# Performance work log

Hardware: AMD Instinct MI355X
Metric: run time of the kernel (lower is better)

## Reference

```python
import jax, jax.numpy as jnp
import numpy as np

BETA = 0.001  # init kwarg beta
S, K = 32768, 32  # segments x candidates-per-segment (uniform segments)


def setup_inputs() -> dict:
    key = jax.random.key(0)
    logits = jax.random.normal(key, (S * K,), dtype=jnp.float32)
    # cumulative segment offsets: [0, K, 2K, ..., S*K]  (uniform ragged structure)
    k_lens = jnp.arange(S + 1, dtype=jnp.int32) * K
    return {"logits": logits, "k_lens": k_lens}


def reference(logits, k_lens):
    # Static shapes derived from array shapes (uniform segments).
    n_seg = k_lens.shape[0] - 1              # S
    seg_len = logits.shape[0] // n_seg       # K
    seg = logits.reshape(n_seg, seg_len)     # [S, K]
    # torch.combinations(arange(K), 2) == upper-triangular index pairs (i < j)
    i_idx, j_idx = jnp.triu_indices(seg_len, k=1)  # each [P], P = K*(K-1)/2
    pos = seg[:, i_idx]                      # [S, P]
    neg = seg[:, j_idx]                      # [S, P]
    l2 = 0.5 * (pos * pos - neg * neg)
    # per-segment loss: -mean(logsigmoid(pos-neg) + beta*l2)
    loss = -jnp.mean(jax.nn.log_sigmoid(pos - neg) + BETA * l2, axis=1)  # [S]
    return loss  # reduction=None -> stacked per-segment losses
```

## Files before the change

### kernel.cpp

```cpp
#include <hip/hip_runtime.h>


constexpr int K = 32;
constexpr int ITERS = 16;

struct alignas(16) Tab {
    unsigned int A[64][4];
    unsigned int B[64][4];
};
constexpr Tab make_tab() {
    Tab t{};
    unsigned char ai[512] = {}, aj[512] = {};
    int p = 0;
    for (int i = 0; i < K; ++i)
        for (int j = i + 1; j < K; ++j) { ai[p] = (unsigned char)(i * 4); aj[p] = (unsigned char)(j * 4); ++p; }
    for (int it = 0; it < ITERS; ++it)
        for (int l = 0; l < 32; ++l) {
            const int s = it * 32 + l;
            for (int half = 0; half < 2; ++half) {
                const int lane = l + 32 * half;
                const unsigned int a = ai[s] + 128u * half;
                const unsigned int b = aj[s] + 128u * half;
                t.A[lane][it >> 2] |= a << ((it & 3) * 8);
                t.B[lane][it >> 2] |= b << ((it & 3) * 8);
            }
        }
    return t;
}
__constant__ Tab TAB = make_tab();

__device__ __forceinline__ float bperm(int byteaddr, float v) {
    return __int_as_float(__builtin_amdgcn_ds_bpermute(byteaddr, __float_as_int(v)));
}

#if __has_builtin(__builtin_amdgcn_exp2f)
#define FAST_EXP2(x) __builtin_amdgcn_exp2f(x)
#else
#define FAST_EXP2(x) exp2f(x)
#endif
#if __has_builtin(__builtin_amdgcn_logf)
#define FAST_LOG2(x) __builtin_amdgcn_logf(x)
#else
#define FAST_LOG2(x) log2f(x)
#endif

__global__ __launch_bounds__(1024) void rmloss_kernel(
        const float* __restrict__ logits, float* __restrict__ out, int n_seg) {
    const int lane = threadIdx.x & 63;
    const int wave = blockIdx.x * 16 + (threadIdx.x >> 6);
    const int seg0 = wave * 2;
    if (seg0 >= n_seg) return;

    const long long gidx = (long long)wave * 64 + lane;
    float x = 0.0f;
    if (gidx < (long long)n_seg * K) x = logits[gidx];

    constexpr float LOG2E = 1.4426950408889634f;
    constexpr float LN2   = 0.6931471805599453f;
    const float y = x * LOG2E;

    const uint4 wa = *reinterpret_cast<const uint4*>(&TAB.A[lane][0]);
    const uint4 wb = *reinterpret_cast<const uint4*>(&TAB.B[lane][0]);
    const unsigned int Aw[4] = {wa.x, wa.y, wa.z, wa.w};
    const unsigned int Bw[4] = {wb.x, wb.y, wb.z, wb.w};

    float acc = 0.0f;
#pragma unroll
    for (int it = 0; it < ITERS; ++it) {
        const int w = it >> 2, sh = (it & 3) * 8;
        const int ai = (int)((Aw[w] >> sh) & 0xffu);
        const int aj = (int)((Bw[w] >> sh) & 0xffu);
        const float yi = bperm(ai, y);
        const float yj = bperm(aj, y);
        acc += FAST_LOG2(1.0f + FAST_EXP2(yj - yi));
    }

    const int k = lane & 31;
    float r = LN2 * (acc - 0.5f) - 0.0005f * (float)(31 - 2 * k) * x * x;

#pragma unroll
    for (int off = 16; off; off >>= 1) r += __shfl_xor(r, off, 64);

    if ((lane & 31) == 0) {
        const int seg = seg0 + (lane >> 5);
        if (seg < n_seg) out[seg] = r * (1.0f / 496.0f);
    }
}

extern "C" void kernel_launch(void* const* d_in, const int* in_sizes, int n_in,
                              void* d_out, int out_size, void* d_ws, size_t ws_size,
                              hipStream_t stream) {
    const float* logits = (const float*)d_in[0];
    const int n_seg = in_sizes[1] - 1;
    float* out = (float*)d_out;
    const int segs_per_block = 32;
    const int blocks = (n_seg + segs_per_block - 1) / segs_per_block;
    rmloss_kernel<<<blocks, 1024, 0, stream>>>(logits, out, n_seg);
}
```

Before: 61.99 us.

## Replace pairwise bpermute loop with XOR-swizzle product of exponentials

Rewrites the per-pair softplus sum as, for each lane, the product over all 31 XOR partners of (1 + e_partner * f_self), where e = 2^y and f = 2^-y. One log2 is taken per batch of eight factors, and a linear correction term in x accounts for the symmetric double counting. This removes the constant-memory index tables and the two bpermutes per pair, and cuts the transcendental count to roughly four logs plus two exps per lane. Neighbours now come from ds_swizzle in XOR mode, and the final reduction uses swizzle instead of shfl. The risk is overflow or underflow of the products for large logits, since eight factors of exp(x_j - x_i) are multiplied before the log is taken.

After: 58.10 us. 6.3% less time.

```diff
diff --git a/kernel.cpp b/kernel.cpp
--- a/kernel.cpp
+++ b/kernel.cpp
@@ -2,36 +2,6 @@
 
 
 constexpr int K = 32;
-constexpr int ITERS = 16;
-
-struct alignas(16) Tab {
-    unsigned int A[64][4];
-    unsigned int B[64][4];
-};
-constexpr Tab make_tab() {
-    Tab t{};
-    unsigned char ai[512] = {}, aj[512] = {};
-    int p = 0;
-    for (int i = 0; i < K; ++i)
-        for (int j = i + 1; j < K; ++j) { ai[p] = (unsigned char)(i * 4); aj[p] = (unsigned char)(j * 4); ++p; }
-    for (int it = 0; it < ITERS; ++it)
-        for (int l = 0; l < 32; ++l) {
-            const int s = it * 32 + l;
-            for (int half = 0; half < 2; ++half) {
-                const int lane = l + 32 * half;
-                const unsigned int a = ai[s] + 128u * half;
-                const unsigned int b = aj[s] + 128u * half;
-                t.A[lane][it >> 2] |= a << ((it & 3) * 8);
-                t.B[lane][it >> 2] |= b << ((it & 3) * 8);
-            }
-        }
-    return t;
-}
-__constant__ Tab TAB = make_tab();
-
-__device__ __forceinline__ float bperm(int byteaddr, float v) {
-    return __int_as_float(__builtin_amdgcn_ds_bpermute(byteaddr, __float_as_int(v)));
-}
 
 #if __has_builtin(__builtin_amdgcn_exp2f)
 #define FAST_EXP2(x) __builtin_amdgcn_exp2f(x)
@@ -43,6 +13,17 @@
 #else
 #define FAST_LOG2(x) log2f(x)
 #endif
+
+#define XSTEP(M)                                                          \
+    do {                                                                  \
+        const float ep = __int_as_float(__builtin_amdgcn_ds_swizzle(      \
+            __float_as_int(e), ((M) << 10) | 0x1f));                      \
+        prod *= fmaf(ep, f, 1.0f);                                        \
+    } while (0)
+
+#define RSTEP(M)                                                          \
+    r += __int_as_float(__builtin_amdgcn_ds_swizzle(                      \
+        __float_as_int(r), ((M) << 10) | 0x1f))
 
 __global__ __launch_bounds__(1024) void rmloss_kernel(
         const float* __restrict__ logits, float* __restrict__ out, int n_seg) {
@@ -58,28 +39,28 @@
     constexpr float LOG2E = 1.4426950408889634f;
     constexpr float LN2   = 0.6931471805599453f;
     const float y = x * LOG2E;
+    const float e = FAST_EXP2(y);
+    const float f = FAST_EXP2(-y);
 
-    const uint4 wa = *reinterpret_cast<const uint4*>(&TAB.A[lane][0]);
-    const uint4 wb = *reinterpret_cast<const uint4*>(&TAB.B[lane][0]);
-    const unsigned int Aw[4] = {wa.x, wa.y, wa.z, wa.w};
-    const unsigned int Bw[4] = {wb.x, wb.y, wb.z, wb.w};
+    float acc, prod = 1.0f;
+    XSTEP(1);  XSTEP(2);  XSTEP(3);  XSTEP(4);
+    XSTEP(5);  XSTEP(6);  XSTEP(7);  XSTEP(8);
+    acc = FAST_LOG2(prod); prod = 1.0f;
+    XSTEP(9);  XSTEP(10); XSTEP(11); XSTEP(12);
+    XSTEP(13); XSTEP(14); XSTEP(15); XSTEP(16);
+    acc += FAST_LOG2(prod); prod = 1.0f;
+    XSTEP(17); XSTEP(18); XSTEP(19); XSTEP(20);
+    XSTEP(21); XSTEP(22); XSTEP(23); XSTEP(24);
+    acc += FAST_LOG2(prod); prod = 1.0f;
+    XSTEP(25); XSTEP(26); XSTEP(27); XSTEP(28);
+    XSTEP(29); XSTEP(30); XSTEP(31);
+    acc += FAST_LOG2(prod);
 
-    float acc = 0.0f;
-#pragma unroll
-    for (int it = 0; it < ITERS; ++it) {
-        const int w = it >> 2, sh = (it & 3) * 8;
-        const int ai = (int)((Aw[w] >> sh) & 0xffu);
-        const int aj = (int)((Bw[w] >> sh) & 0xffu);
-        const float yi = bperm(ai, y);
-        const float yj = bperm(aj, y);
-        acc += FAST_LOG2(1.0f + FAST_EXP2(yj - yi));
-    }
+    const int   k = lane & 31;
+    const float c = (float)(2 * k - 31);
+    float r = fmaf(0.5f * LN2, acc, c * x * fmaf(0.0005f, x, 0.5f));
 
-    const int k = lane & 31;
-    float r = LN2 * (acc - 0.5f) - 0.0005f * (float)(31 - 2 * k) * x * x;
-
-#pragma unroll
-    for (int off = 16; off; off >>= 1) r += __shfl_xor(r, off, 64);
+    RSTEP(16); RSTEP(8); RSTEP(4); RSTEP(2); RSTEP(1);
 
     if ((lane & 31) == 0) {
         const int seg = seg0 + (lane >> 5);
```
